# Performance work log

Measured on AMD Instinct MI355X. Metric: run time of the kernel, lower is better.

## Reference

```python
import jax, jax.numpy as jnp
import numpy as np

N_NODES = 1_000_000
N_EDGES = 16_000_000
NUM_GRAPHS = 64
LATENT = 128
LAMBDA_LAP = 0.1
LAMBDA_DRIFT = 0.01
LAMBDA_ARAP = 0.1
BETA_WARMUP = 10
BETA_FINAL = 1.0


def setup_inputs() -> dict:
    key = jax.random.key(0)
    k1, k2, k3, k4, k5, k6 = jax.random.split(key, 6)
    return {
        "pred_output": jax.random.normal(k1, (N_NODES, 2), dtype=jnp.float32),
        "target": jax.random.normal(k2, (N_NODES, 2), dtype=jnp.float32),
        "edge_index": jax.random.randint(k3, (2, N_EDGES), 0, N_NODES, dtype=jnp.int32),
        "batch_indices": jnp.sort(jax.random.randint(k4, (N_NODES,), 0, NUM_GRAPHS, dtype=jnp.int32)),
        "mu": jax.random.normal(k5, (NUM_GRAPHS, LATENT), dtype=jnp.float32),
        "logvar": jax.random.normal(k6, (NUM_GRAPHS, LATENT), dtype=jnp.float32),
        "epoch": 5,
    }


def reference(pred_output, target, edge_index, batch_indices, mu, logvar, epoch):
    # reconstruction: MSE, mean over all elements
    recon = jnp.mean((pred_output - target) ** 2)

    # edge gather once; laplacian and ARAP reuse the same diff tensor
    i, j = edge_index[0], edge_index[1]
    diff = pred_output[i] - pred_output[j]                 # [E, 2]
    lap = jnp.sum(diff ** 2) / edge_index.shape[1]

    # drift suppression: per-graph mean displacement via segment_sum
    ones = jnp.ones((pred_output.shape[0],), dtype=pred_output.dtype)
    sums = jax.ops.segment_sum(pred_output, batch_indices, num_segments=NUM_GRAPHS)
    counts = jax.ops.segment_sum(ones, batch_indices, num_segments=NUM_GRAPHS)
    means = sums / counts[:, None]                         # [G, 2]
    drift = jnp.sum(means ** 2) / NUM_GRAPHS

    # ARAP: unbiased variance of edge lengths (torch.var default ddof=1)
    edge_len = jnp.sqrt(jnp.sum(diff ** 2, axis=1))        # [E]
    arap = jnp.var(edge_len, ddof=1)

    # KL divergence, mean over graphs
    kl = jnp.mean(-0.5 * jnp.sum(1.0 + logvar - mu ** 2 - jnp.exp(logvar), axis=1))

    # beta warmup (epoch is a static python int)
    beta = (epoch / BETA_WARMUP) * BETA_FINAL if epoch < BETA_WARMUP else BETA_FINAL

    total = recon + LAMBDA_LAP * lap + LAMBDA_DRIFT * drift + LAMBDA_ARAP * arap + beta * kl
    return total
```

## Files before the change

### kernel.cpp

```cpp
#include <hip/hip_runtime.h>
#include <hip/hip_fp16.h>
#include <math.h>

#define N_NODES    1000000
#define N_EDGES    16000000
#define NUM_GRAPHS 64
#define LATENT     128

#define WS_DOUBLES 200
#define PACKED_OFFSET 2048

typedef int vint4 __attribute__((ext_vector_type(4)));

__global__ void init_ws(double* ws) {
    int t = blockIdx.x * blockDim.x + threadIdx.x;
    if (t < WS_DOUBLES) ws[t] = 0.0;
}

__global__ void node_kl_pass(const float2* __restrict__ pred,
                             const float2* __restrict__ targ,
                             const int*    __restrict__ batch,
                             const float*  __restrict__ mu,
                             const float*  __restrict__ logvar,
                             double* __restrict__ ws,
                             unsigned* __restrict__ packed) {
    __shared__ float sgx[NUM_GRAPHS];
    __shared__ float sgy[NUM_GRAPHS];
    __shared__ int   scnt[NUM_GRAPHS];
    __shared__ double smem[8];

    for (int g = threadIdx.x; g < NUM_GRAPHS; g += blockDim.x) {
        sgx[g] = 0.f; sgy[g] = 0.f; scnt[g] = 0;
    }
    __syncthreads();

    float recon = 0.f;
    const int idx = blockIdx.x * blockDim.x + threadIdx.x;
    const int stride = gridDim.x * blockDim.x;
    for (int n = idx; n < N_NODES; n += stride) {
        float2 p = pred[n];
        float2 t = targ[n];
        float dx = p.x - t.x, dy = p.y - t.y;
        recon += dx * dx + dy * dy;

        if (packed) {
            __half2 h = __floats2half2_rn(p.x, p.y);
            packed[n] = *reinterpret_cast<unsigned*>(&h);
        }

        int b = batch[n];
        unsigned long long act = __ballot(1);
        int b0 = __shfl(b, 0);
        bool fast = (act == ~0ull) && (__ballot(b == b0) == act);
        if (fast) {
            float sx = p.x, sy = p.y;
            #pragma unroll
            for (int off = 32; off > 0; off >>= 1) {
                sx += __shfl_xor(sx, off);
                sy += __shfl_xor(sy, off);
            }
            if ((threadIdx.x & 63) == 0) {
                atomicAdd(&sgx[b0], sx);
                atomicAdd(&sgy[b0], sy);
                atomicAdd(&scnt[b0], 64);
            }
        } else {
            atomicAdd(&sgx[b], p.x);
            atomicAdd(&sgy[b], p.y);
            atomicAdd(&scnt[b], 1);
        }
    }

    double r = (double)recon;
    #pragma unroll
    for (int off = 32; off > 0; off >>= 1) r += __shfl_down(r, off);
    const int lane = threadIdx.x & 63;
    const int wid  = threadIdx.x >> 6;
    if (lane == 0) smem[wid] = r;
    __syncthreads();
    if (threadIdx.x == 0) {
        double tot = 0.0;
        const int nw = blockDim.x >> 6;
        for (int w = 0; w < nw; ++w) tot += smem[w];
        atomicAdd(&ws[0], tot);
    }

    for (int g = threadIdx.x; g < NUM_GRAPHS; g += blockDim.x) {
        if (scnt[g] != 0) {
            atomicAdd(&ws[4 + g],   (double)sgx[g]);
            atomicAdd(&ws[68 + g],  (double)sgy[g]);
            atomicAdd(&ws[132 + g], (double)scnt[g]);
        }
    }

    if (blockIdx.x == 0) {
        double s = 0.0;
        for (int t = threadIdx.x; t < NUM_GRAPHS * LATENT; t += blockDim.x) {
            float m = mu[t], lv = logvar[t];
            s += (double)(1.0f + lv - m * m - expf(lv));
        }
        #pragma unroll
        for (int off = 32; off > 0; off >>= 1) s += __shfl_down(s, off);
        __syncthreads();
        if (lane == 0) smem[wid] = s;
        __syncthreads();
        if (threadIdx.x == 0) {
            double tot = 0.0;
            const int nw = blockDim.x >> 6;
            for (int w = 0; w < nw; ++w) tot += smem[w];
            atomicAdd(&ws[3], tot);
        }
    }
}

__device__ __forceinline__ void edge_flush(float s1, float s2, double* ws,
                                           double* smem1, double* smem2) {
    double r1 = (double)s1, r2 = (double)s2;
    #pragma unroll
    for (int off = 32; off > 0; off >>= 1) {
        r1 += __shfl_down(r1, off);
        r2 += __shfl_down(r2, off);
    }
    const int lane = threadIdx.x & 63;
    const int wid  = threadIdx.x >> 6;
    if (lane == 0) { smem1[wid] = r1; smem2[wid] = r2; }
    __syncthreads();
    if (threadIdx.x == 0) {
        double t1 = 0.0, t2 = 0.0;
        const int nw = blockDim.x >> 6;
        for (int w = 0; w < nw; ++w) { t1 += smem1[w]; t2 += smem2[w]; }
        atomicAdd(&ws[1], t1);
        atomicAdd(&ws[2], t2);
    }
}

__device__ __forceinline__ vint4 ld_stream_x4(const vint4* p) {
    vint4 r;
    asm volatile("global_load_dwordx4 %0, %1, off sc0 sc1 nt"
                 : "=v"(r) : "v"(p) : "memory");
    return r;
}

__device__ __forceinline__ void acc_pair(unsigned pa, unsigned pb,
                                         float& s1, float& s2) {
    __half2 ha = *reinterpret_cast<__half2*>(&pa);
    __half2 hb = *reinterpret_cast<__half2*>(&pb);
    float2 fa = __half22float2(ha);
    float2 fb = __half22float2(hb);
    float dx = fa.x - fb.x, dy = fa.y - fb.y;
    float l2 = dx * dx + dy * dy;
    s2 += l2;
    s1 += sqrtf(l2);
}

__global__ void edge_pass_packed(const unsigned* __restrict__ packed,
                                 const int* __restrict__ ei,
                                 double* __restrict__ ws) {
    __shared__ double smem1[8];
    __shared__ double smem2[8];

    float s1 = 0.f, s2 = 0.f;
    const int gid = blockIdx.x * blockDim.x + threadIdx.x;
    const int stride = gridDim.x * blockDim.x;
    const int ngroups = N_EDGES / 8;
    const vint4* eia = (const vint4*)ei;
    const vint4* eib = (const vint4*)(ei + N_EDGES);

    int g = gid;
    if (g < ngroups) {
        vint4 a0 = ld_stream_x4(eia + 2 * g);
        vint4 a1 = ld_stream_x4(eia + 2 * g + 1);
        vint4 b0 = ld_stream_x4(eib + 2 * g);
        vint4 b1 = ld_stream_x4(eib + 2 * g + 1);
        asm volatile("s_waitcnt vmcnt(0)"
                     : "+v"(a0), "+v"(a1), "+v"(b0), "+v"(b1) :: "memory");
        __builtin_amdgcn_sched_barrier(0);
        while (true) {
            const int gn = g + stride;
            const bool more = gn < ngroups;
            vint4 a0n = {0,0,0,0}, a1n = {0,0,0,0};
            vint4 b0n = {0,0,0,0}, b1n = {0,0,0,0};
            if (more) {
                a0n = ld_stream_x4(eia + 2 * gn);
                a1n = ld_stream_x4(eia + 2 * gn + 1);
                b0n = ld_stream_x4(eib + 2 * gn);
                b1n = ld_stream_x4(eib + 2 * gn + 1);
            }

            unsigned qa0 = packed[a0.x], qb0 = packed[b0.x];
            unsigned qa1 = packed[a0.y], qb1 = packed[b0.y];
            unsigned qa2 = packed[a0.z], qb2 = packed[b0.z];
            unsigned qa3 = packed[a0.w], qb3 = packed[b0.w];
            unsigned qa4 = packed[a1.x], qb4 = packed[b1.x];
            unsigned qa5 = packed[a1.y], qb5 = packed[b1.y];
            unsigned qa6 = packed[a1.z], qb6 = packed[b1.z];
            unsigned qa7 = packed[a1.w], qb7 = packed[b1.w];

            acc_pair(qa0, qb0, s1, s2);
            acc_pair(qa1, qb1, s1, s2);
            acc_pair(qa2, qb2, s1, s2);
            acc_pair(qa3, qb3, s1, s2);
            acc_pair(qa4, qb4, s1, s2);
            acc_pair(qa5, qb5, s1, s2);
            acc_pair(qa6, qb6, s1, s2);
            acc_pair(qa7, qb7, s1, s2);

            if (!more) break;
            asm volatile("s_waitcnt vmcnt(0)"
                         : "+v"(a0n), "+v"(a1n), "+v"(b0n), "+v"(b1n) :: "memory");
            __builtin_amdgcn_sched_barrier(0);
            g = gn; a0 = a0n; a1 = a1n; b0 = b0n; b1 = b1n;
        }
    }
    asm volatile("s_waitcnt vmcnt(0)" ::: "memory");
    edge_flush(s1, s2, ws, smem1, smem2);
}

__global__ void edge_pass_f32(const float2* __restrict__ pred,
                              const int* __restrict__ ei,
                              double* __restrict__ ws) {
    __shared__ double smem1[8];
    __shared__ double smem2[8];

    float s1 = 0.f, s2 = 0.f;
    const int idx = blockIdx.x * blockDim.x + threadIdx.x;
    const int stride = gridDim.x * blockDim.x;
    for (int e = idx; e < N_EDGES; e += stride) {
        int i = ei[e];
        int j = ei[N_EDGES + e];
        float2 pi = pred[i];
        float2 pj = pred[j];
        float dx = pi.x - pj.x, dy = pi.y - pj.y;
        float l2 = dx * dx + dy * dy;
        s2 += l2;
        s1 += sqrtf(l2);
    }
    edge_flush(s1, s2, ws, smem1, smem2);
}

__global__ void finalize(const double* __restrict__ ws,
                         const int* __restrict__ epoch_p,
                         float* __restrict__ out) {
    double recon = ws[0] / (2.0 * (double)N_NODES);
    double S1 = ws[1], S2 = ws[2];
    double lap  = S2 / (double)N_EDGES;
    double arap = (S2 - S1 * S1 / (double)N_EDGES) / ((double)N_EDGES - 1.0);
    double drift = 0.0;
    for (int g = 0; g < NUM_GRAPHS; ++g) {
        double c  = ws[132 + g];
        double mx = ws[4 + g] / c;
        double my = ws[68 + g] / c;
        drift += mx * mx + my * my;
    }
    drift /= (double)NUM_GRAPHS;
    double kl = -0.5 * ws[3] / (double)NUM_GRAPHS;
    int epoch = *epoch_p;
    double beta = (epoch < 10) ? ((double)epoch / 10.0) : 1.0;
    out[0] = (float)(recon + 0.1 * lap + 0.01 * drift + 0.1 * arap + beta * kl);
}

extern "C" void kernel_launch(void* const* d_in, const int* in_sizes, int n_in,
                              void* d_out, int out_size, void* d_ws, size_t ws_size,
                              hipStream_t stream) {
    const float2* pred   = (const float2*)d_in[0];
    const float2* targ   = (const float2*)d_in[1];
    const int*    ei     = (const int*)d_in[2];
    const int*    batch  = (const int*)d_in[3];
    const float*  mu     = (const float*)d_in[4];
    const float*  logvar = (const float*)d_in[5];
    const int*    epoch  = (const int*)d_in[6];
    float* out = (float*)d_out;
    double* ws = (double*)d_ws;

    const bool use_packed = ws_size >= (size_t)PACKED_OFFSET + 4ull * N_NODES;
    unsigned* packed = use_packed
        ? (unsigned*)((char*)d_ws + PACKED_OFFSET) : (unsigned*)nullptr;

    init_ws<<<1, 256, 0, stream>>>(ws);
    node_kl_pass<<<1024, 256, 0, stream>>>(pred, targ, batch, mu, logvar, ws, packed);
    if (use_packed)
        edge_pass_packed<<<2048, 256, 0, stream>>>(packed, ei, ws);
    else
        edge_pass_f32<<<2048, 256, 0, stream>>>(pred, ei, ws);
    finalize<<<1, 1, 0, stream>>>(ws, epoch, out);
}
```

Before: 379.8 us.

## Shard global atomics into shadow slots, chunk nodes per wave, simplify edge prefetch

Global double atomics for the node and edge reductions are spread across several shadow copies, keyed by block index, and summed in finalize, to reduce contention on single addresses. The node pass now gives each wave a contiguous chunk and keeps a per-lane running per-graph sum, flushing to shared memory only when the graph id changes. This replaces the per-iteration ballot and shuffle logic, and the node grid is doubled. The edge pass drops the inline-asm 8-edge double-buffered streaming loads in favour of 4-edge groups with compiler nontemporal loads, which may give up some memory-level parallelism. The workspace layout changes, and the new path needs a larger workspace.

```diff
diff --git a/kernel.cpp b/kernel.cpp
--- a/kernel.cpp
+++ b/kernel.cpp
@@ -7,14 +7,21 @@
 #define NUM_GRAPHS 64
 #define LATENT     128
 
-#define WS_DOUBLES 200
-#define PACKED_OFFSET 2048
+#define SH_BASE        8
+#define SH_STRIDE      200
+#define NSHADOW_BIG    8
+#define EDGE_SH_BASE   1608
+#define EDGE_NSHADOW   16
+#define WS_DOUBLES_TOT 1736
+#define WS_DOUBLES_LEGACY 208
+#define PACKED_OFFSET_BIG    16384
+#define PACKED_OFFSET_LEGACY 2048
 
 typedef int vint4 __attribute__((ext_vector_type(4)));
 
-__global__ void init_ws(double* ws) {
+__global__ void init_ws(double* ws, int n) {
     int t = blockIdx.x * blockDim.x + threadIdx.x;
-    if (t < WS_DOUBLES) ws[t] = 0.0;
+    if (t < n) ws[t] = 0.0;
 }
 
 __global__ void node_kl_pass(const float2* __restrict__ pred,
@@ -23,7 +30,8 @@
                              const float*  __restrict__ mu,
                              const float*  __restrict__ logvar,
                              double* __restrict__ ws,
-                             unsigned* __restrict__ packed) {
+                             unsigned* __restrict__ packed,
+                             int ns) {
     __shared__ float sgx[NUM_GRAPHS];
     __shared__ float sgy[NUM_GRAPHS];
     __shared__ int   scnt[NUM_GRAPHS];
@@ -34,62 +42,68 @@
     }
     __syncthreads();
 
+    double* shbase = ws + SH_BASE + (size_t)(blockIdx.x & (ns - 1)) * SH_STRIDE;
+
+    const int lane   = threadIdx.x & 63;
+    const int wid    = threadIdx.x >> 6;
+    const int nwaves = (gridDim.x * blockDim.x) >> 6;
+    const int gwave  = (blockIdx.x * blockDim.x + threadIdx.x) >> 6;
+    const int chunk  = (N_NODES + nwaves - 1) / nwaves;
+    const int start  = gwave * chunk;
+    const int end    = (start + chunk < N_NODES) ? (start + chunk) : N_NODES;
+
     float recon = 0.f;
-    const int idx = blockIdx.x * blockDim.x + threadIdx.x;
-    const int stride = gridDim.x * blockDim.x;
-    for (int n = idx; n < N_NODES; n += stride) {
-        float2 p = pred[n];
-        float2 t = targ[n];
-        float dx = p.x - t.x, dy = p.y - t.y;
-        recon += dx * dx + dy * dy;
-
-        if (packed) {
-            __half2 h = __floats2half2_rn(p.x, p.y);
-            packed[n] = *reinterpret_cast<unsigned*>(&h);
-        }
-
-        int b = batch[n];
-        unsigned long long act = __ballot(1);
-        int b0 = __shfl(b, 0);
-        bool fast = (act == ~0ull) && (__ballot(b == b0) == act);
-        if (fast) {
-            float sx = p.x, sy = p.y;
-            #pragma unroll
-            for (int off = 32; off > 0; off >>= 1) {
-                sx += __shfl_xor(sx, off);
-                sy += __shfl_xor(sy, off);
-            }
-            if ((threadIdx.x & 63) == 0) {
-                atomicAdd(&sgx[b0], sx);
-                atomicAdd(&sgy[b0], sy);
-                atomicAdd(&scnt[b0], 64);
-            }
-        } else {
-            atomicAdd(&sgx[b], p.x);
-            atomicAdd(&sgy[b], p.y);
-            atomicAdd(&scnt[b], 1);
-        }
+    float sx = 0.f, sy = 0.f;
+    int   cnt = 0, bcur = -1;
+
+    for (int n0 = start; n0 < end; n0 += 64) {
+        const int n = n0 + lane;
+        if (n < end) {
+            float2 p = pred[n];
+            float2 t = targ[n];
+            float dx = p.x - t.x, dy = p.y - t.y;
+            recon += dx * dx + dy * dy;
+
+            if (packed) {
+                __half2 h = __floats2half2_rn(p.x, p.y);
+                packed[n] = *reinterpret_cast<unsigned*>(&h);
+            }
+
+            int b = batch[n];
+            if (b != bcur) {
+                if (cnt != 0) {
+                    atomicAdd(&sgx[bcur], sx);
+                    atomicAdd(&sgy[bcur], sy);
+                    atomicAdd(&scnt[bcur], cnt);
+                }
+                bcur = b; sx = 0.f; sy = 0.f; cnt = 0;
+            }
+            sx += p.x; sy += p.y; ++cnt;
+        }
+    }
+    if (cnt != 0) {
+        atomicAdd(&sgx[bcur], sx);
+        atomicAdd(&sgy[bcur], sy);
+        atomicAdd(&scnt[bcur], cnt);
     }
 
     double r = (double)recon;
     #pragma unroll
     for (int off = 32; off > 0; off >>= 1) r += __shfl_down(r, off);
-    const int lane = threadIdx.x & 63;
-    const int wid  = threadIdx.x >> 6;
     if (lane == 0) smem[wid] = r;
     __syncthreads();
     if (threadIdx.x == 0) {
         double tot = 0.0;
         const int nw = blockDim.x >> 6;
         for (int w = 0; w < nw; ++w) tot += smem[w];
-        atomicAdd(&ws[0], tot);
+        atomicAdd(&shbase[0], tot);
     }
 
     for (int g = threadIdx.x; g < NUM_GRAPHS; g += blockDim.x) {
         if (scnt[g] != 0) {
-            atomicAdd(&ws[4 + g],   (double)sgx[g]);
-            atomicAdd(&ws[68 + g],  (double)sgy[g]);
-            atomicAdd(&ws[132 + g], (double)scnt[g]);
+            atomicAdd(&shbase[2 + g],   (double)sgx[g]);
+            atomicAdd(&shbase[66 + g],  (double)sgy[g]);
+            atomicAdd(&shbase[130 + g], (double)scnt[g]);
         }
     }
 
@@ -108,12 +122,13 @@
             double tot = 0.0;
             const int nw = blockDim.x >> 6;
             for (int w = 0; w < nw; ++w) tot += smem[w];
-            atomicAdd(&ws[3], tot);
+            atomicAdd(&shbase[1], tot);
         }
     }
 }
 
 __device__ __forceinline__ void edge_flush(float s1, float s2, double* ws,
+                                           int edge_mode,
                                            double* smem1, double* smem2) {
     double r1 = (double)s1, r2 = (double)s2;
     #pragma unroll
@@ -129,96 +144,97 @@
         double t1 = 0.0, t2 = 0.0;
         const int nw = blockDim.x >> 6;
         for (int w = 0; w < nw; ++w) { t1 += smem1[w]; t2 += smem2[w]; }
-        atomicAdd(&ws[1], t1);
-        atomicAdd(&ws[2], t2);
-    }
-}
-
-__device__ __forceinline__ vint4 ld_stream_x4(const vint4* p) {
-    vint4 r;
-    asm volatile("global_load_dwordx4 %0, %1, off sc0 sc1 nt"
-                 : "=v"(r) : "v"(p) : "memory");
-    return r;
-}
-
-__device__ __forceinline__ void acc_pair(unsigned pa, unsigned pb,
-                                         float& s1, float& s2) {
-    __half2 ha = *reinterpret_cast<__half2*>(&pa);
-    __half2 hb = *reinterpret_cast<__half2*>(&pb);
-    float2 fa = __half22float2(ha);
-    float2 fb = __half22float2(hb);
-    float dx = fa.x - fb.x, dy = fa.y - fb.y;
-    float l2 = dx * dx + dy * dy;
-    s2 += l2;
-    s1 += sqrtf(l2);
+        if (edge_mode) {
+            const int sh = blockIdx.x & (EDGE_NSHADOW - 1);
+            atomicAdd(&ws[EDGE_SH_BASE + sh * 8 + 0], t1);
+            atomicAdd(&ws[EDGE_SH_BASE + sh * 8 + 1], t2);
+        } else {
+            atomicAdd(&ws[1], t1);
+            atomicAdd(&ws[2], t2);
+        }
+    }
 }
 
 __global__ void edge_pass_packed(const unsigned* __restrict__ packed,
                                  const int* __restrict__ ei,
-                                 double* __restrict__ ws) {
+                                 double* __restrict__ ws,
+                                 int edge_mode) {
     __shared__ double smem1[8];
     __shared__ double smem2[8];
 
     float s1 = 0.f, s2 = 0.f;
     const int gid = blockIdx.x * blockDim.x + threadIdx.x;
     const int stride = gridDim.x * blockDim.x;
-    const int ngroups = N_EDGES / 8;
+    const int ngroups = N_EDGES / 4;
     const vint4* eia = (const vint4*)ei;
     const vint4* eib = (const vint4*)(ei + N_EDGES);
 
     int g = gid;
     if (g < ngroups) {
-        vint4 a0 = ld_stream_x4(eia + 2 * g);
-        vint4 a1 = ld_stream_x4(eia + 2 * g + 1);
-        vint4 b0 = ld_stream_x4(eib + 2 * g);
-        vint4 b1 = ld_stream_x4(eib + 2 * g + 1);
-        asm volatile("s_waitcnt vmcnt(0)"
-                     : "+v"(a0), "+v"(a1), "+v"(b0), "+v"(b1) :: "memory");
-        __builtin_amdgcn_sched_barrier(0);
+        vint4 a = __builtin_nontemporal_load(eia + g);
+        vint4 b = __builtin_nontemporal_load(eib + g);
         while (true) {
+            unsigned pa0 = packed[a.x], pb0 = packed[b.x];
+            unsigned pa1 = packed[a.y], pb1 = packed[b.y];
+            unsigned pa2 = packed[a.z], pb2 = packed[b.z];
+            unsigned pa3 = packed[a.w], pb3 = packed[b.w];
+
             const int gn = g + stride;
             const bool more = gn < ngroups;
-            vint4 a0n = {0,0,0,0}, a1n = {0,0,0,0};
-            vint4 b0n = {0,0,0,0}, b1n = {0,0,0,0};
+            vint4 an = {0, 0, 0, 0}, bn = {0, 0, 0, 0};
             if (more) {
-                a0n = ld_stream_x4(eia + 2 * gn);
-                a1n = ld_stream_x4(eia + 2 * gn + 1);
-                b0n = ld_stream_x4(eib + 2 * gn);
-                b1n = ld_stream_x4(eib + 2 * gn + 1);
-            }
-
-            unsigned qa0 = packed[a0.x], qb0 = packed[b0.x];
-            unsigned qa1 = packed[a0.y], qb1 = packed[b0.y];
-            unsigned qa2 = packed[a0.z], qb2 = packed[b0.z];
-            unsigned qa3 = packed[a0.w], qb3 = packed[b0.w];
-            unsigned qa4 = packed[a1.x], qb4 = packed[b1.x];
-            unsigned qa5 = packed[a1.y], qb5 = packed[b1.y];
-            unsigned qa6 = packed[a1.z], qb6 = packed[b1.z];
-            unsigned qa7 = packed[a1.w], qb7 = packed[b1.w];
-
-            acc_pair(qa0, qb0, s1, s2);
-            acc_pair(qa1, qb1, s1, s2);
-            acc_pair(qa2, qb2, s1, s2);
-            acc_pair(qa3, qb3, s1, s2);
-            acc_pair(qa4, qb4, s1, s2);
-            acc_pair(qa5, qb5, s1, s2);
-            acc_pair(qa6, qb6, s1, s2);
-            acc_pair(qa7, qb7, s1, s2);
+                an = __builtin_nontemporal_load(eia + gn);
+                bn = __builtin_nontemporal_load(eib + gn);
+            }
+
+            {
+                __half2 ha = *reinterpret_cast<__half2*>(&pa0);
+                __half2 hb = *reinterpret_cast<__half2*>(&pb0);
+                float2 fa = __half22float2(ha);
+                float2 fb = __half22float2(hb);
+                float dx = fa.x - fb.x, dy = fa.y - fb.y;
+                float l2 = dx * dx + dy * dy;
+                s2 += l2; s1 += sqrtf(l2);
+            }
+            {
+                __half2 ha = *reinterpret_cast<__half2*>(&pa1);
+                __half2 hb = *reinterpret_cast<__half2*>(&pb1);
+                float2 fa = __half22float2(ha);
+                float2 fb = __half22float2(hb);
+                float dx = fa.x - fb.x, dy = fa.y - fb.y;
+                float l2 = dx * dx + dy * dy;
+                s2 += l2; s1 += sqrtf(l2);
+            }
+            {
+                __half2 ha = *reinterpret_cast<__half2*>(&pa2);
+                __half2 hb = *reinterpret_cast<__half2*>(&pb2);
+                float2 fa = __half22float2(ha);
+                float2 fb = __half22float2(hb);
+                float dx = fa.x - fb.x, dy = fa.y - fb.y;
+                float l2 = dx * dx + dy * dy;
+                s2 += l2; s1 += sqrtf(l2);
+            }
+            {
+                __half2 ha = *reinterpret_cast<__half2*>(&pa3);
+                __half2 hb = *reinterpret_cast<__half2*>(&pb3);
+                float2 fa = __half22float2(ha);
+                float2 fb = __half22float2(hb);
+                float dx = fa.x - fb.x, dy = fa.y - fb.y;
+                float l2 = dx * dx + dy * dy;
+                s2 += l2; s1 += sqrtf(l2);
+            }
 
             if (!more) break;
-            asm volatile("s_waitcnt vmcnt(0)"
-                         : "+v"(a0n), "+v"(a1n), "+v"(b0n), "+v"(b1n) :: "memory");
-            __builtin_amdgcn_sched_barrier(0);
-            g = gn; a0 = a0n; a1 = a1n; b0 = b0n; b1 = b1n;
-        }
-    }
-    asm volatile("s_waitcnt vmcnt(0)" ::: "memory");
-    edge_flush(s1, s2, ws, smem1, smem2);
+            g = gn; a = an; b = bn;
+        }
+    }
+    edge_flush(s1, s2, ws, edge_mode, smem1, smem2);
 }
 
 __global__ void edge_pass_f32(const float2* __restrict__ pred,
                               const int* __restrict__ ei,
-                              double* __restrict__ ws) {
+                              double* __restrict__ ws,
+                              int edge_mode) {
     __shared__ double smem1[8];
     __shared__ double smem2[8];
 
@@ -235,25 +251,44 @@
         s2 += l2;
         s1 += sqrtf(l2);
     }
-    edge_flush(s1, s2, ws, smem1, smem2);
+    edge_flush(s1, s2, ws, edge_mode, smem1, smem2);
 }
 
 __global__ void finalize(const double* __restrict__ ws,
                          const int* __restrict__ epoch_p,
-                         float* __restrict__ out) {
-    double recon = ws[0] / (2.0 * (double)N_NODES);
-    double S1 = ws[1], S2 = ws[2];
+                         float* __restrict__ out,
+                         int ns, int edge_mode) {
+    double recon_sum = 0.0, kl_sum = 0.0;
+    for (int s = 0; s < ns; ++s) {
+        recon_sum += ws[SH_BASE + s * SH_STRIDE + 0];
+        kl_sum    += ws[SH_BASE + s * SH_STRIDE + 1];
+    }
+    double S1, S2;
+    if (edge_mode) {
+        S1 = 0.0; S2 = 0.0;
+        for (int s = 0; s < EDGE_NSHADOW; ++s) {
+            S1 += ws[EDGE_SH_BASE + s * 8 + 0];
+            S2 += ws[EDGE_SH_BASE + s * 8 + 1];
+        }
+    } else {
+        S1 = ws[1]; S2 = ws[2];
+    }
+    double recon = recon_sum / (2.0 * (double)N_NODES);
     double lap  = S2 / (double)N_EDGES;
     double arap = (S2 - S1 * S1 / (double)N_EDGES) / ((double)N_EDGES - 1.0);
     double drift = 0.0;
     for (int g = 0; g < NUM_GRAPHS; ++g) {
-        double c  = ws[132 + g];
-        double mx = ws[4 + g] / c;
-        double my = ws[68 + g] / c;
+        double c = 0.0, sx = 0.0, sy = 0.0;
+        for (int s = 0; s < ns; ++s) {
+            c  += ws[SH_BASE + s * SH_STRIDE + 130 + g];
+            sx += ws[SH_BASE + s * SH_STRIDE + 2 + g];
+            sy += ws[SH_BASE + s * SH_STRIDE + 66 + g];
+        }
+        double mx = sx / c, my = sy / c;
         drift += mx * mx + my * my;
     }
     drift /= (double)NUM_GRAPHS;
-    double kl = -0.5 * ws[3] / (double)NUM_GRAPHS;
+    double kl = -0.5 * kl_sum / (double)NUM_GRAPHS;
     int epoch = *epoch_p;
     double beta = (epoch < 10) ? ((double)epoch / 10.0) : 1.0;
     out[0] = (float)(recon + 0.1 * lap + 0.01 * drift + 0.1 * arap + beta * kl);
@@ -272,15 +307,27 @@
     float* out = (float*)d_out;
     double* ws = (double*)d_ws;
 
-    const bool use_packed = ws_size >= (size_t)PACKED_OFFSET + 4ull * N_NODES;
-    unsigned* packed = use_packed
-        ? (unsigned*)((char*)d_ws + PACKED_OFFSET) : (unsigned*)nullptr;
-
-    init_ws<<<1, 256, 0, stream>>>(ws);
-    node_kl_pass<<<1024, 256, 0, stream>>>(pred, targ, batch, mu, logvar, ws, packed);
-    if (use_packed)
-        edge_pass_packed<<<2048, 256, 0, stream>>>(packed, ei, ws);
+    const size_t packed_bytes = 4ull * N_NODES;
+    int ns, edge_mode;
+    unsigned* packed;
+    if (ws_size >= (size_t)PACKED_OFFSET_BIG + packed_bytes) {
+        ns = NSHADOW_BIG; edge_mode = 1;
+        packed = (unsigned*)((char*)d_ws + PACKED_OFFSET_BIG);
+    } else if (ws_size >= (size_t)PACKED_OFFSET_LEGACY + packed_bytes) {
+        ns = 1; edge_mode = 0;
+        packed = (unsigned*)((char*)d_ws + PACKED_OFFSET_LEGACY);
+    } else {
+        ns = 1; edge_mode = 0;
+        packed = nullptr;
+    }
+    const int nz = edge_mode ? WS_DOUBLES_TOT : WS_DOUBLES_LEGACY;
+
+    init_ws<<<(nz + 255) / 256, 256, 0, stream>>>(ws, nz);
+    node_kl_pass<<<2048, 256, 0, stream>>>(pred, targ, batch, mu, logvar, ws,
+                                           packed, ns);
+    if (packed)
+        edge_pass_packed<<<2048, 256, 0, stream>>>(packed, ei, ws, edge_mode);
     else
-        edge_pass_f32<<<2048, 256, 0, stream>>>(pred, ei, ws);
-    finalize<<<1, 1, 0, stream>>>(ws, epoch, out);
-}
+        edge_pass_f32<<<2048, 256, 0, stream>>>(pred, ei, ws, edge_mode);
+    finalize<<<1, 1, 0, stream>>>(ws, epoch, out, ns, edge_mode);
+}
```

New measurement: 394.0 us. 1.04x slower.
